# Kernel optimization log

Measured on AMD Instinct MI355X. Metric: run time of the kernel, lower is better.

Reference implementation:

```python
import jax, jax.numpy as jnp
import numpy as np

NUM_TOKENS = 4096
LATENT_DIM = 256
BETA = 0.25
TEMPERATURE = 1.0  # temp_init buffer value
EPS_TEMP = 1e-6


def setup_inputs() -> dict:
    key = jax.random.key(0)
    k1, k2 = jax.random.split(key)
    latent = jax.random.normal(k1, (4, 2048, LATENT_DIM), dtype=jnp.float32)
    cb = jax.random.normal(k2, (NUM_TOKENS, LATENT_DIM), dtype=jnp.float32)
    # module normalizes codebook rows at init
    codebook = cb / jnp.linalg.norm(cb, axis=-1, keepdims=True)
    return {"latent": latent, "codebook": codebook}


def _l2norm(x):
    return x / jnp.clip(jnp.linalg.norm(x, axis=-1, keepdims=True), 1e-12)


def reference(latent, codebook):
    B, S, D = latent.shape
    flat = latent.reshape(-1, D)                       # [N, D]
    # cosine similarity via normalized matmul
    ln = _l2norm(flat)
    cn = _l2norm(codebook)
    cosine_sim = jnp.einsum('nd,kd->nk', ln, cn)       # [N, K]
    distances = 2.0 - 2.0 * cosine_sim
    scaled = distances / jnp.maximum(TEMPERATURE, EPS_TEMP)
    soft_assign = jax.nn.softmax(-scaled, axis=-1)     # [N, K]
    indices = jnp.argmax(soft_assign, axis=-1)         # [N]
    hard_assign = jax.nn.one_hot(indices, NUM_TOKENS, dtype=jnp.float32)
    # straight-through soft->hard assignment
    assign = hard_assign + soft_assign - jax.lax.stop_gradient(soft_assign)

    selected_cosine_sim = jnp.take_along_axis(cosine_sim, indices[:, None], axis=1).mean()

    # codebook pairwise euclidean diagnostics (off-diagonal mean / min)
    sq = jnp.sum(codebook * codebook, axis=-1)         # [K]
    d2 = sq[:, None] + sq[None, :] - 2.0 * (codebook @ codebook.T)
    cdist = jnp.sqrt(jnp.clip(d2, 0.0))                # [K, K]
    K = NUM_TOKENS
    off_sum = jnp.sum(cdist) - jnp.sum(jnp.diagonal(cdist))
    avg_euclidean = off_sum / (K * (K - 1))
    eye = jnp.eye(K, dtype=bool)
    min_euclidean = jnp.min(jnp.where(eye, jnp.inf, cdist))

    quantized = (assign @ codebook).reshape(B, S, D)
    commitment_loss = BETA * jnp.mean((jax.lax.stop_gradient(latent) - quantized) ** 2)
    codebook_loss = jnp.mean((latent - jax.lax.stop_gradient(quantized)) ** 2)
    quantized = latent + jax.lax.stop_gradient(quantized - latent)

    avg_probs = jnp.mean(hard_assign, axis=0)
    perplexity = jnp.exp(-jnp.sum(avg_probs * jnp.log(avg_probs + 1e-10)))

    return (quantized, indices, commitment_loss, codebook_loss, perplexity,
            selected_cosine_sim, avg_euclidean, min_euclidean)
```

## Files before the change

kernel.cpp:

```cpp
#include <hip/hip_runtime.h>
#include <hip/hip_bf16.h>
#include <math.h>

#define NTOK 8192
#define DIM 256
#define KCB 4096
#define NCB (KCB / 128)
#define NKEY 4
#define NKROW (NCB * NKEY)
#define DELTA 0.08f
#define GTIE 2e-6
#define MAXC 16
#define NPAIRB (NCB * (NCB + 1) / 2)
#define NSCOB (NCB * (NTOK / 128))

typedef unsigned long long ull;
typedef unsigned short ushort;
typedef __attribute__((ext_vector_type(8))) short shortx8;
typedef __attribute__((ext_vector_type(4))) float floatx4;
typedef const __attribute__((address_space(1))) void* gas_cp;
typedef __attribute__((address_space(3))) void* las_p;

__device__ __forceinline__ unsigned f2ord(float f) {
    unsigned u = __float_as_uint(f);
    return (u & 0x80000000u) ? ~u : (u | 0x80000000u);
}
__device__ __forceinline__ float ord2f(unsigned u) {
    unsigned b = (u & 0x80000000u) ? (u & 0x7FFFFFFFu) : ~u;
    return __uint_as_float(b);
}
__device__ __forceinline__ ushort f2bf(float f) {
    unsigned u = __float_as_uint(f);
    unsigned r = u + 0x7FFFu + ((u >> 16) & 1u);
    return (ushort)(r >> 16);
}

union TileSmem {
    struct { ushort a[128][64]; ushort b[128][64]; } t;
    unsigned keys[128][67];
    struct { float rs[256]; float rm[256]; } red;
};

__device__ __forceinline__ void stage_tile4(const ushort* __restrict__ gA,
                                            const ushort* __restrict__ gB,
                                            ushort (*la)[64], ushort (*lb)[64],
                                            int wave, int lane, int kk) {
    int p = lane & 7;
    int rsub = lane >> 3;
    int kc = p ^ rsub;
    const ushort* sa = gA + (size_t)(wave * 32 + rsub) * DIM + kk + kc * 8;
    const ushort* sb = gB + (size_t)(wave * 32 + rsub) * DIM + kk + kc * 8;
#pragma unroll
    for (int c = 0; c < 4; ++c) {
        __builtin_amdgcn_global_load_lds((gas_cp)(sa + (size_t)(c * 8) * DIM),
                                         (las_p)&la[wave * 32 + c * 8][0], 16, 0, 0);
        __builtin_amdgcn_global_load_lds((gas_cp)(sb + (size_t)(c * 8) * DIM),
                                         (las_p)&lb[wave * 32 + c * 8][0], 16, 0, 0);
    }
}
__device__ __forceinline__ shortx8 frag_read(const ushort (*lds)[64], int row,
                                             int lc) {
    return *(const shortx8*)&lds[row][(lc ^ (row & 7)) * 8];
}

__device__ __forceinline__ float np_combine(const float* racc) {
    float h0 = __fadd_rn(__fadd_rn(__fadd_rn(racc[0], racc[1]), __fadd_rn(racc[2], racc[3])),
                         __fadd_rn(__fadd_rn(racc[4], racc[5]), __fadd_rn(racc[6], racc[7])));
    float h1 = __fadd_rn(__fadd_rn(__fadd_rn(racc[8], racc[9]), __fadd_rn(racc[10], racc[11])),
                         __fadd_rn(__fadd_rn(racc[12], racc[13]), __fadd_rn(racc[14], racc[15])));
    float s = __fadd_rn(h0, h1);
    return fmaxf(sqrtf(s), 1e-12f);
}

__global__ __launch_bounds__(256) void prep(const float* __restrict__ lat,
                                            const float* __restrict__ cb,
                                            float* __restrict__ nrml,
                                            float* __restrict__ nrmc,
                                            ushort* __restrict__ latbf,
                                            ushort* __restrict__ cnbf,
                                            ushort* __restrict__ cbbf,
                                            float* __restrict__ sq,
                                            unsigned* __restrict__ counts) {
    int bid = blockIdx.x, t = threadIdx.x;
    if (bid < NTOK) {
        int n = bid;
        if (n < KCB / 256) counts[n * 256 + t] = 0u;
        const float* row = lat + (size_t)n * DIM;
        latbf[(size_t)n * DIM + t] = f2bf(row[t]);
        __shared__ float racc[16];
        if (t < 16) {
            int h = t >> 3, j = t & 7;
            const float* p = row + h * 128;
            float r = __fmul_rn(p[j], p[j]);
#pragma unroll 1
            for (int i = 8; i < 128; i += 8)
                r = __fadd_rn(r, __fmul_rn(p[i + j], p[i + j]));
            racc[t] = r;
        }
        __syncthreads();
        if (t == 0) nrml[n] = np_combine(racc);
    } else {
        int n = bid - NTOK;
        __shared__ float racc2[16];
        __shared__ double dacc[16];
        __shared__ float snrm;
        const float* row = cb + (size_t)n * DIM;
        if (t < 16) {
            int h = t >> 3, j = t & 7;
            const float* p = row + h * 128;
            float r = __fmul_rn(p[j], p[j]);
            double ds = 0.0;
#pragma unroll 1
            for (int i = 8; i < 128; i += 8)
                r = __fadd_rn(r, __fmul_rn(p[i + j], p[i + j]));
#pragma unroll 1
            for (int i = 0; i < 128; i += 8) { double v = (double)p[i + j]; ds += v * v; }
            racc2[t] = r; dacc[t] = ds;
        }
        __syncthreads();
        if (t == 0) {
            float nr = np_combine(racc2);
            snrm = nr; nrmc[n] = nr;
            double ds = 0.0;
            for (int i = 0; i < 16; ++i) ds += dacc[i];
            sq[n] = (float)ds;
        }
        __syncthreads();
        float c = row[t];
        cnbf[(size_t)n * DIM + t] = f2bf(c / snrm);
        cbbf[(size_t)n * DIM + t] = f2bf(c);
    }
}

__global__ __launch_bounds__(256, 3) void gemms(const ushort* __restrict__ latbf,
                                                const ushort* __restrict__ cnbf,
                                                const ushort* __restrict__ cbbf,
                                                const float* __restrict__ sq,
                                                unsigned* __restrict__ keysw,
                                                float* __restrict__ psumw,
                                                unsigned* __restrict__ pminw) {
    __shared__ TileSmem sm;
    int tid = threadIdx.x;
    int wave = tid >> 6, lane = tid & 63;
    int quad = lane >> 4, l15 = lane & 15;
    int wr = wave >> 1, wc = wave & 1;
    bool isScore = blockIdx.x < NSCOB;
    int rowBase, colBase, tri = 0;
    const ushort *gA, *gB;
    if (isScore) {
        int cbk = blockIdx.x & (NCB - 1);
        int rbk = blockIdx.x >> 5;
        rowBase = rbk * 128; colBase = cbk * 128;
        gA = latbf + (size_t)rowBase * DIM;
        gB = cnbf + (size_t)colBase * DIM;
    } else {
        tri = blockIdx.x - NSCOB;
        int a = (int)((sqrtf(8.f * tri + 1.f) - 1.f) * 0.5f);
        while ((a + 1) * (a + 2) / 2 <= tri) ++a;
        while (a * (a + 1) / 2 > tri) --a;
        int b = tri - a * (a + 1) / 2;
        rowBase = b * 128; colBase = a * 128;
        gA = cbbf + (size_t)rowBase * DIM;
        gB = cbbf + (size_t)colBase * DIM;
    }
    floatx4 acc[4][4];
#pragma unroll
    for (int m = 0; m < 4; ++m)
#pragma unroll
        for (int n = 0; n < 4; ++n) acc[m][n] = (floatx4){0.f, 0.f, 0.f, 0.f};
#pragma unroll 1
    for (int kk = 0; kk < DIM; kk += 64) {
        __syncthreads();
        stage_tile4(gA, gB, sm.t.a, sm.t.b, wave, lane, kk);
        __syncthreads();
#pragma unroll
        for (int s = 0; s < 2; ++s) {
            shortx8 af[4], bfv[4];
#pragma unroll
            for (int mt = 0; mt < 4; ++mt)
                af[mt] = frag_read(sm.t.a, wr * 64 + mt * 16 + l15, s * 4 + quad);
#pragma unroll
            for (int nt = 0; nt < 4; ++nt)
                bfv[nt] = frag_read(sm.t.b, wc * 64 + nt * 16 + l15, s * 4 + quad);
#pragma unroll
            for (int mt = 0; mt < 4; ++mt)
#pragma unroll
                for (int nt = 0; nt < 4; ++nt)
                    acc[mt][nt] = __builtin_amdgcn_mfma_f32_16x16x32_bf16(
                        af[mt], bfv[nt], acc[mt][nt], 0, 0, 0);
        }
    }
    __syncthreads();
    if (isScore) {
        unsigned colp2[4];
#pragma unroll
        for (int nt = 0; nt < 4; ++nt)
            colp2[nt] = 0x80000000u | (4095u - (unsigned)(colBase + wc * 64 + nt * 16 + l15));
#pragma unroll
        for (int mt = 0; mt < 4; ++mt)
#pragma unroll
            for (int reg = 0; reg < 4; ++reg) {
                unsigned b1 = 0u, b2 = 0u;
#pragma unroll
                for (int nt = 0; nt < 4; ++nt) {
                    unsigned key = (__float_as_uint(fmaxf(acc[mt][nt][reg], 0.f)) & 0x7FFFF000u)
                                   | colp2[nt];
                    unsigned lo = min(key, b1);
                    b1 = max(key, b1);
                    b2 = max(lo, b2);
                }
                int row = wr * 64 + mt * 16 + quad * 4 + reg;
                uint2 kv; kv.x = b1; kv.y = b2;
                *(uint2*)&sm.keys[row][(wc * 16 + l15) * 2] = kv;
            }
        __syncthreads();
        {
            int prow = tid >> 1, ph = tid & 1;
            unsigned a0 = 0, a1 = 0, a2 = 0, a3 = 0;
#pragma unroll
            for (int j = 0; j < 8; ++j) {
                uint4 v4 = *(const uint4*)&sm.keys[prow][ph * 32 + j * 4];
                unsigned vs[4] = {v4.x, v4.y, v4.z, v4.w};
#pragma unroll
                for (int q = 0; q < 4; ++q) {
                    unsigned v = vs[q];
                    unsigned n0 = min(v, a0); a0 = max(v, a0);
                    unsigned n1 = min(n0, a1); a1 = max(n0, a1);
                    unsigned n2 = min(n1, a2); a2 = max(n1, a2);
                    a3 = max(n2, a3);
                }
            }
            uint4 mine; mine.x = a0; mine.y = a1; mine.z = a2; mine.w = a3;
            *(uint4*)&sm.keys[prow][ph * 32] = mine;
            __syncthreads();
            if (ph == 0) {
                uint4 o4 = *(const uint4*)&sm.keys[prow][32];
                unsigned vs[4] = {o4.x, o4.y, o4.z, o4.w};
#pragma unroll
                for (int q = 0; q < 4; ++q) {
                    unsigned v = vs[q];
                    unsigned n0 = min(v, a0); a0 = max(v, a0);
                    unsigned n1 = min(n0, a1); a1 = max(n0, a1);
                    unsigned n2 = min(n1, a2); a2 = max(n1, a2);
                    a3 = max(n2, a3);
                }
                size_t base = (size_t)(rowBase + prow) * NKROW + (blockIdx.x & (NCB - 1)) * NKEY;
                uint4 o; o.x = a0; o.y = a1; o.z = a2; o.w = a3;
                *(uint4*)&keysw[base] = o;
            }
        }
    } else {
        float lsum = 0.f, lmin = INFINITY;
#pragma unroll
        for (int mt = 0; mt < 4; ++mt)
#pragma unroll
            for (int reg = 0; reg < 4; ++reg) {
                int i = rowBase + wr * 64 + mt * 16 + quad * 4 + reg;
                float sqi = sq[i];
#pragma unroll
                for (int nt = 0; nt < 4; ++nt) {
                    int j = colBase + wc * 64 + nt * 16 + l15;
                    float d2 = sqi + sq[j] - 2.0f * acc[mt][nt][reg];
                    float d = sqrtf(fmaxf(d2, 0.0f));
                    bool use = i < j;
                    lsum += use ? d : 0.f;
                    lmin = fminf(lmin, use ? d : INFINITY);
                }
            }
        sm.red.rs[tid] = lsum; sm.red.rm[tid] = lmin; __syncthreads();
        for (int s = 128; s > 0; s >>= 1) {
            if (tid < s) {
                sm.red.rs[tid] += sm.red.rs[tid + s];
                sm.red.rm[tid] = fminf(sm.red.rm[tid], sm.red.rm[tid + s]);
            }
            __syncthreads();
        }
        if (tid == 0) { psumw[tri] = sm.red.rs[0]; pminw[tri] = f2ord(sm.red.rm[0]); }
    }
}

__global__ __launch_bounds__(256) void argmax_resolve(const float* __restrict__ lat,
                                                      const float* __restrict__ cb,
                                                      const float* __restrict__ nrml,
                                                      const float* __restrict__ nrmc,
                                                      const unsigned* __restrict__ keysw,
                                                      float* __restrict__ outidx,
                                                      float* __restrict__ outq,
                                                      unsigned* __restrict__ counts,
                                                      float* __restrict__ selw,
                                                      float* __restrict__ msew) {
    __shared__ int scand[4][MAXC];
    __shared__ double sc64[4][MAXC];
    int wid = threadIdx.x >> 6, lane = threadIdx.x & 63;
    int n = blockIdx.x * 4 + wid;
    const unsigned* kr = keysw + (size_t)n * NKROW;
    uint2 kv = *(const uint2*)(kr + lane * 2);
    unsigned m = max(kv.x, kv.y);
#pragma unroll
    for (int off = 1; off < 64; off <<= 1) {
        unsigned o = __shfl_xor(m, off, 64);
        m = max(m, o);
    }
    float v1 = ord2f(m & 0xFFFFF000u);
    float thresh = v1 - DELTA;
    bool p0 = ord2f(kv.x & 0xFFFFF000u) >= thresh;
    bool p1 = ord2f(kv.y & 0xFFFFF000u) >= thresh;
    ull b0 = __ballot(p0), b1 = __ballot(p1);
    int below0 = __builtin_amdgcn_mbcnt_hi((unsigned)(b0 >> 32),
                 __builtin_amdgcn_mbcnt_lo((unsigned)b0, 0));
    int below1 = __builtin_amdgcn_mbcnt_hi((unsigned)(b1 >> 32),
                 __builtin_amdgcn_mbcnt_lo((unsigned)b1, 0));
    int base1 = __popcll(b0);
    int nc = base1 + __popcll(b1);
    if (p0 && below0 < MAXC)
        scand[wid][below0] = 4095 - (int)(kv.x & 0xFFFu);
    if (p1 && base1 + below1 < MAXC)
        scand[wid][base1 + below1] = 4095 - (int)(kv.y & 0xFFFu);
    nc = nc < MAXC ? nc : MAXC;
    __threadfence_block();
    float nx = nrml[n];
    int d0 = lane * 4;
    float4 xv = *(const float4*)(lat + (size_t)n * DIM + d0);
    int idx; float selcos;
    if (nc <= 1) {
        idx = 4095 - (int)(m & 0xFFFu);
        selcos = v1 / nx;
    } else {
        float la0 = xv.x / nx, la1 = xv.y / nx, la2 = xv.z / nx, la3 = xv.w / nx;
        for (int c = 0; c < nc; ++c) {
            int k = scand[wid][c];
            float nk = nrmc[k];
            float4 cv = *(const float4*)(cb + (size_t)k * DIM + d0);
            double part = (double)(cv.x / nk) * la0 + (double)(cv.y / nk) * la1 +
                          (double)(cv.z / nk) * la2 + (double)(cv.w / nk) * la3;
#pragma unroll
            for (int off = 1; off < 64; off <<= 1) part += __shfl_xor(part, off, 64);
            if (lane == 0) sc64[wid][c] = part;
        }
        __threadfence_block();
        double best64 = -1e300;
        for (int c = 0; c < nc; ++c) best64 = fmax(best64, sc64[wid][c]);
        int nrisk = 0;
        for (int c = 0; c < nc; ++c) if (sc64[wid][c] >= best64 - GTIE) ++nrisk;
        if (nrisk == 1) {
            idx = 0x7FFFFFFF; selcos = 0.f;
            for (int c = 0; c < nc; ++c)
                if (sc64[wid][c] >= best64 - GTIE) { idx = scand[wid][c]; selcos = (float)sc64[wid][c]; }
        } else {
            ull keyf = 0ull, keym = 0ull;
            if (lane < nc && sc64[wid][lane] >= best64 - GTIE) {
                int k = scand[wid][lane];
                const float* cr = cb + (size_t)k * DIM;
                const float* x = lat + (size_t)n * DIM;
                float nk = nrmc[k];
                float af = 0.f, am = 0.f;
                for (int d = 0; d < DIM; ++d) {
                    float la = x[d] / nx;
                    float cv = cr[d] / nk;
                    af = fmaf(la, cv, af);
                    am = __fadd_rn(am, __fmul_rn(la, cv));
                }
                float df = __fsub_rn(2.0f, __fmul_rn(2.0f, af));
                float dm = __fsub_rn(2.0f, __fmul_rn(2.0f, am));
                keyf = ((ull)(0xFFFFFFFFu - f2ord(df)) << 32) | (ull)(0xFFFFFFFFu - (unsigned)k);
                keym = ((ull)(0xFFFFFFFFu - f2ord(dm)) << 32) | (ull)(0xFFFFFFFFu - (unsigned)k);
            }
#pragma unroll
            for (int off = 1; off < 64; off <<= 1) {
                ull of = __shfl_xor(keyf, off, 64);
                ull om = __shfl_xor(keym, off, 64);
                keyf = of > keyf ? of : keyf;
                keym = om > keym ? om : keym;
            }
            int colf = (int)(0xFFFFFFFFu - (unsigned)(keyf & 0xFFFFFFFFull));
            int colm = (int)(0xFFFFFFFFu - (unsigned)(keym & 0xFFFFFFFFull));
            idx = colf < colm ? colf : colm;
            selcos = 0.f;
            for (int c = 0; c < nc; ++c)
                if (scand[wid][c] == idx) selcos = (float)sc64[wid][c];
        }
    }
    float4 qv = *(const float4*)(cb + (size_t)idx * DIM + d0);
    *(float4*)(outq + (size_t)n * DIM + d0) = qv;
    float dx = xv.x - qv.x, dy = xv.y - qv.y, dz = xv.z - qv.z, dw = xv.w - qv.w;
    float msep = fmaf(dx, dx, fmaf(dy, dy, fmaf(dz, dz, dw * dw)));
#pragma unroll
    for (int off = 1; off < 64; off <<= 1) msep += __shfl_xor(msep, off, 64);
    if (lane == 0) {
        outidx[n] = (float)idx;
        atomicAdd(&counts[idx], 1u);
        selw[n] = selcos;
        msew[n] = msep;
    }
}

__global__ void finalize(const unsigned* __restrict__ counts,
                         const float* __restrict__ selw,
                         const float* __restrict__ msew,
                         const float* __restrict__ psumw,
                         const unsigned* __restrict__ pminw,
                         float* __restrict__ outs) {
    int t = threadIdx.x;
    __shared__ float red[256];
    float h = 0.f;
    for (int k = t; k < KCB; k += 256) {
        float p = (float)counts[k] * (1.0f / (float)NTOK);
        h += p * logf(p + 1e-10f);
    }
    red[t] = h; __syncthreads();
    for (int s = 128; s > 0; s >>= 1) { if (t < s) red[t] += red[t + s]; __syncthreads(); }
    float entNeg = red[0];
    __syncthreads();
    float ssel = 0.f;
    for (int k = t; k < NTOK; k += 256) ssel += selw[k];
    red[t] = ssel; __syncthreads();
    for (int s = 128; s > 0; s >>= 1) { if (t < s) red[t] += red[t + s]; __syncthreads(); }
    float selSum = red[0];
    __syncthreads();
    float sm = 0.f;
    for (int k = t; k < NTOK; k += 256) sm += msew[k];
    red[t] = sm; __syncthreads();
    for (int s = 128; s > 0; s >>= 1) { if (t < s) red[t] += red[t + s]; __syncthreads(); }
    float mseSum = red[0];
    __syncthreads();
    float ps = 0.f;
    for (int k = t; k < NPAIRB; k += 256) ps += psumw[k];
    red[t] = ps; __syncthreads();
    for (int s = 128; s > 0; s >>= 1) { if (t < s) red[t] += red[t + s]; __syncthreads(); }
    float pairSum = red[0];
    __syncthreads();
    unsigned pm = 0xFFFFFFFFu;
    for (int k = t; k < NPAIRB; k += 256) pm = min(pm, pminw[k]);
    ((unsigned*)red)[t] = pm; __syncthreads();
    for (int s = 128; s > 0; s >>= 1) {
        if (t < s) ((unsigned*)red)[t] = min(((unsigned*)red)[t], ((unsigned*)red)[t + s]);
        __syncthreads();
    }
    unsigned pairMin = ((unsigned*)red)[0];
    if (t == 0) {
        float mse = mseSum / (float)(NTOK * DIM);
        outs[0] = 0.25f * mse;
        outs[1] = mse;
        outs[2] = expf(-entNeg);
        outs[3] = selSum / (float)NTOK;
        outs[4] = pairSum * 2.0f / ((float)KCB * (float)(KCB - 1));
        outs[5] = ord2f(pairMin);
    }
}

extern "C" void kernel_launch(void* const* d_in, const int* in_sizes, int n_in,
                              void* d_out, int out_size, void* d_ws, size_t ws_size,
                              hipStream_t stream) {
    const float* latent = (const float*)d_in[0];
    const float* codebook = (const float*)d_in[1];
    float* out = (float*)d_out;
    float* outq = out;
    float* outidx = out + (size_t)NTOK * DIM;
    float* outs = outidx + NTOK;

    unsigned* keysw = (unsigned*)d_ws;
    ushort* latbf = (ushort*)(keysw + (size_t)NKROW * NTOK);
    ushort* cnbf = latbf + (size_t)NTOK * DIM;
    ushort* cbbf = cnbf + (size_t)KCB * DIM;
    float* nrml = (float*)(cbbf + (size_t)KCB * DIM);
    float* nrmc = nrml + NTOK;
    float* sq = nrmc + KCB;
    unsigned* counts = (unsigned*)(sq + KCB);
    float* selw = (float*)(counts + KCB);
    float* msew = selw + NTOK;
    float* psumw = msew + NTOK;
    unsigned* pminw = (unsigned*)(psumw + NPAIRB);

    hipLaunchKernelGGL(prep, dim3(NTOK + KCB), dim3(256), 0, stream,
                       latent, codebook, nrml, nrmc, latbf, cnbf, cbbf, sq, counts);
    hipLaunchKernelGGL(gemms, dim3(NSCOB + NPAIRB), dim3(256), 0, stream,
                       latbf, cnbf, cbbf, sq, keysw, psumw, pminw);
    hipLaunchKernelGGL(argmax_resolve, dim3(NTOK / 4), dim3(256), 0, stream,
                       latent, codebook, nrml, nrmc, keysw, outidx, outq, counts, selw, msew);
    hipLaunchKernelGGL(finalize, dim3(1), dim3(256), 0, stream, counts, selw, msew, psumw, pminw, outs);
}
```

Baseline: 173.0 us.

## Double-buffer GEMM LDS tiles and process one row per wave in prep

The GEMM main loop now uses two LDS tile buffers. The next K-slice is prefetched with global_load_lds while MFMAs run on the current one, and the two syncthreads per step become one waitcnt plus barrier. This doubles the LDS tile footprint, so the occupancy hint is lowered from 3 to 2 blocks per CU. The prep kernel now handles one row per wave, using float4 loads, shuffle reductions and no shared-memory barriers, which cuts its grid by a factor of four.

```diff
diff --git a/kernel.cpp b/kernel.cpp
--- a/kernel.cpp
+++ b/kernel.cpp
@@ -36,7 +36,7 @@
 }
 
 union TileSmem {
-    struct { ushort a[128][64]; ushort b[128][64]; } t;
+    struct { ushort a[128][64]; ushort b[128][64]; } t[2];
     unsigned keys[128][67];
     struct { float rs[256]; float rm[256]; } red;
 };
@@ -61,15 +61,6 @@
 __device__ __forceinline__ shortx8 frag_read(const ushort (*lds)[64], int row,
                                              int lc) {
     return *(const shortx8*)&lds[row][(lc ^ (row & 7)) * 8];
-}
-
-__device__ __forceinline__ float np_combine(const float* racc) {
-    float h0 = __fadd_rn(__fadd_rn(__fadd_rn(racc[0], racc[1]), __fadd_rn(racc[2], racc[3])),
-                         __fadd_rn(__fadd_rn(racc[4], racc[5]), __fadd_rn(racc[6], racc[7])));
-    float h1 = __fadd_rn(__fadd_rn(__fadd_rn(racc[8], racc[9]), __fadd_rn(racc[10], racc[11])),
-                         __fadd_rn(__fadd_rn(racc[12], racc[13]), __fadd_rn(racc[14], racc[15])));
-    float s = __fadd_rn(h0, h1);
-    return fmaxf(sqrtf(s), 1e-12f);
 }
 
 __global__ __launch_bounds__(256) void prep(const float* __restrict__ lat,
@@ -82,57 +73,66 @@
                                             float* __restrict__ sq,
                                             unsigned* __restrict__ counts) {
     int bid = blockIdx.x, t = threadIdx.x;
-    if (bid < NTOK) {
-        int n = bid;
-        if (n < KCB / 256) counts[n * 256 + t] = 0u;
+    int wid = t >> 6, lane = t & 63;
+    int h = (lane >> 3) & 1, j = lane & 7;
+    if (bid < NTOK / 4) {
+        int n = bid * 4 + wid;
+        if (bid < 16) counts[bid * 256 + t] = 0u;
         const float* row = lat + (size_t)n * DIM;
-        latbf[(size_t)n * DIM + t] = f2bf(row[t]);
-        __shared__ float racc[16];
-        if (t < 16) {
-            int h = t >> 3, j = t & 7;
-            const float* p = row + h * 128;
-            float r = __fmul_rn(p[j], p[j]);
+        int d0 = lane * 4;
+        float4 xv = *(const float4*)(row + d0);
+        ushort4 bv;
+        bv.x = f2bf(xv.x); bv.y = f2bf(xv.y); bv.z = f2bf(xv.z); bv.w = f2bf(xv.w);
+        *(ushort4*)(latbf + (size_t)n * DIM + d0) = bv;
+        const float* p = row + h * 128;
+        float r = __fmul_rn(p[j], p[j]);
 #pragma unroll 1
-            for (int i = 8; i < 128; i += 8)
-                r = __fadd_rn(r, __fmul_rn(p[i + j], p[i + j]));
-            racc[t] = r;
-        }
-        __syncthreads();
-        if (t == 0) nrml[n] = np_combine(racc);
+        for (int i = 8; i < 128; i += 8)
+            r = __fadd_rn(r, __fmul_rn(p[i + j], p[i + j]));
+        float v[16];
+#pragma unroll
+        for (int l = 0; l < 16; ++l) v[l] = __shfl(r, l, 64);
+        float h0 = __fadd_rn(__fadd_rn(__fadd_rn(v[0], v[1]), __fadd_rn(v[2], v[3])),
+                             __fadd_rn(__fadd_rn(v[4], v[5]), __fadd_rn(v[6], v[7])));
+        float h1 = __fadd_rn(__fadd_rn(__fadd_rn(v[8], v[9]), __fadd_rn(v[10], v[11])),
+                             __fadd_rn(__fadd_rn(v[12], v[13]), __fadd_rn(v[14], v[15])));
+        float nr = fmaxf(sqrtf(__fadd_rn(h0, h1)), 1e-12f);
+        if (lane == 0) nrml[n] = nr;
     } else {
-        int n = bid - NTOK;
-        __shared__ float racc2[16];
-        __shared__ double dacc[16];
-        __shared__ float snrm;
+        int n = (bid - NTOK / 4) * 4 + wid;
         const float* row = cb + (size_t)n * DIM;
-        if (t < 16) {
-            int h = t >> 3, j = t & 7;
-            const float* p = row + h * 128;
-            float r = __fmul_rn(p[j], p[j]);
-            double ds = 0.0;
+        int d0 = lane * 4;
+        float4 xv = *(const float4*)(row + d0);
+        const float* p = row + h * 128;
+        float r = __fmul_rn(p[j], p[j]);
+        double ds = 0.0;
 #pragma unroll 1
-            for (int i = 8; i < 128; i += 8)
-                r = __fadd_rn(r, __fmul_rn(p[i + j], p[i + j]));
+        for (int i = 8; i < 128; i += 8)
+            r = __fadd_rn(r, __fmul_rn(p[i + j], p[i + j]));
 #pragma unroll 1
-            for (int i = 0; i < 128; i += 8) { double v = (double)p[i + j]; ds += v * v; }
-            racc2[t] = r; dacc[t] = ds;
-        }
-        __syncthreads();
-        if (t == 0) {
-            float nr = np_combine(racc2);
-            snrm = nr; nrmc[n] = nr;
-            double ds = 0.0;
-            for (int i = 0; i < 16; ++i) ds += dacc[i];
-            sq[n] = (float)ds;
-        }
-        __syncthreads();
-        float c = row[t];
-        cnbf[(size_t)n * DIM + t] = f2bf(c / snrm);
-        cbbf[(size_t)n * DIM + t] = f2bf(c);
-    }
-}
-
-__global__ __launch_bounds__(256, 3) void gemms(const ushort* __restrict__ latbf,
+        for (int i = 0; i < 128; i += 8) { double vv = (double)p[i + j]; ds += vv * vv; }
+        float v[16];
+#pragma unroll
+        for (int l = 0; l < 16; ++l) v[l] = __shfl(r, l, 64);
+        float h0 = __fadd_rn(__fadd_rn(__fadd_rn(v[0], v[1]), __fadd_rn(v[2], v[3])),
+                             __fadd_rn(__fadd_rn(v[4], v[5]), __fadd_rn(v[6], v[7])));
+        float h1 = __fadd_rn(__fadd_rn(__fadd_rn(v[8], v[9]), __fadd_rn(v[10], v[11])),
+                             __fadd_rn(__fadd_rn(v[12], v[13]), __fadd_rn(v[14], v[15])));
+        float nr = fmaxf(sqrtf(__fadd_rn(h0, h1)), 1e-12f);
+        double dsum = 0.0;
+#pragma unroll 1
+        for (int l = 0; l < 16; ++l) dsum += __shfl(ds, l, 64);
+        if (lane == 0) { nrmc[n] = nr; sq[n] = (float)dsum; }
+        ushort4 cn, cbv;
+        cn.x = f2bf(xv.x / nr); cn.y = f2bf(xv.y / nr);
+        cn.z = f2bf(xv.z / nr); cn.w = f2bf(xv.w / nr);
+        cbv.x = f2bf(xv.x); cbv.y = f2bf(xv.y); cbv.z = f2bf(xv.z); cbv.w = f2bf(xv.w);
+        *(ushort4*)(cnbf + (size_t)n * DIM + d0) = cn;
+        *(ushort4*)(cbbf + (size_t)n * DIM + d0) = cbv;
+    }
+}
+
+__global__ __launch_bounds__(256, 2) void gemms(const ushort* __restrict__ latbf,
                                                 const ushort* __restrict__ cnbf,
                                                 const ushort* __restrict__ cbbf,
                                                 const float* __restrict__ sq,
@@ -168,26 +168,37 @@
     for (int m = 0; m < 4; ++m)
 #pragma unroll
         for (int n = 0; n < 4; ++n) acc[m][n] = (floatx4){0.f, 0.f, 0.f, 0.f};
-#pragma unroll 1
-    for (int kk = 0; kk < DIM; kk += 64) {
-        __syncthreads();
-        stage_tile4(gA, gB, sm.t.a, sm.t.b, wave, lane, kk);
-        __syncthreads();
+
+    stage_tile4(gA, gB, sm.t[0].a, sm.t[0].b, wave, lane, 0);
+    asm volatile("s_waitcnt vmcnt(0)" ::: "memory");
+    __builtin_amdgcn_s_barrier();
+    asm volatile("" ::: "memory");
+#pragma unroll
+    for (int t = 0; t < 4; ++t) {
+        int cur = t & 1;
+        if (t < 3)
+            stage_tile4(gA, gB, sm.t[cur ^ 1].a, sm.t[cur ^ 1].b, wave, lane,
+                        (t + 1) * 64);
 #pragma unroll
         for (int s = 0; s < 2; ++s) {
             shortx8 af[4], bfv[4];
 #pragma unroll
             for (int mt = 0; mt < 4; ++mt)
-                af[mt] = frag_read(sm.t.a, wr * 64 + mt * 16 + l15, s * 4 + quad);
+                af[mt] = frag_read(sm.t[cur].a, wr * 64 + mt * 16 + l15, s * 4 + quad);
 #pragma unroll
             for (int nt = 0; nt < 4; ++nt)
-                bfv[nt] = frag_read(sm.t.b, wc * 64 + nt * 16 + l15, s * 4 + quad);
+                bfv[nt] = frag_read(sm.t[cur].b, wc * 64 + nt * 16 + l15, s * 4 + quad);
 #pragma unroll
             for (int mt = 0; mt < 4; ++mt)
 #pragma unroll
                 for (int nt = 0; nt < 4; ++nt)
                     acc[mt][nt] = __builtin_amdgcn_mfma_f32_16x16x32_bf16(
                         af[mt], bfv[nt], acc[mt][nt], 0, 0, 0);
+        }
+        if (t < 3) {
+            asm volatile("s_waitcnt vmcnt(0)" ::: "memory");
+            __builtin_amdgcn_s_barrier();
+            asm volatile("" ::: "memory");
         }
     }
     __syncthreads();
@@ -218,8 +229,8 @@
             int prow = tid >> 1, ph = tid & 1;
             unsigned a0 = 0, a1 = 0, a2 = 0, a3 = 0;
 #pragma unroll
-            for (int j = 0; j < 8; ++j) {
-                uint4 v4 = *(const uint4*)&sm.keys[prow][ph * 32 + j * 4];
+            for (int j2 = 0; j2 < 8; ++j2) {
+                uint4 v4 = *(const uint4*)&sm.keys[prow][ph * 32 + j2 * 4];
                 unsigned vs[4] = {v4.x, v4.y, v4.z, v4.w};
 #pragma unroll
                 for (int q = 0; q < 4; ++q) {
@@ -259,10 +270,10 @@
                 float sqi = sq[i];
 #pragma unroll
                 for (int nt = 0; nt < 4; ++nt) {
-                    int j = colBase + wc * 64 + nt * 16 + l15;
-                    float d2 = sqi + sq[j] - 2.0f * acc[mt][nt][reg];
+                    int j2 = colBase + wc * 64 + nt * 16 + l15;
+                    float d2 = sqi + sq[j2] - 2.0f * acc[mt][nt][reg];
                     float d = sqrtf(fmaxf(d2, 0.0f));
-                    bool use = i < j;
+                    bool use = i < j2;
                     lsum += use ? d : 0.f;
                     lmin = fminf(lmin, use ? d : INFINITY);
                 }
@@ -471,7 +482,7 @@
     float* psumw = msew + NTOK;
     unsigned* pminw = (unsigned*)(psumw + NPAIRB);
 
-    hipLaunchKernelGGL(prep, dim3(NTOK + KCB), dim3(256), 0, stream,
+    hipLaunchKernelGGL(prep, dim3(NTOK / 4 + KCB / 4), dim3(256), 0, stream,
                        latent, codebook, nrml, nrmc, latbf, cnbf, cbbf, sq, counts);
     hipLaunchKernelGGL(gemms, dim3(NSCOB + NPAIRB), dim3(256), 0, stream,
                        latbf, cnbf, cbbf, sq, keysw, psumw, pminw);
```

New measurement: 167.1 us. 1.04x faster.
